# Optimization experiments

Measured on AMD Instinct MI355X. Metric: run time of the kernel, lower is better.

The kernel has to match this reference:

```python
import jax, jax.numpy as jnp
import numpy as np

SIGMA = 1.5
KSIZE = 3
CROP = 5

def _gaussian_window():
    # matches cv2.getGaussianKernel(3, 1.5): normalized 1D gaussian, outer product
    g = np.exp(-((np.arange(KSIZE) - (KSIZE - 1) / 2.0) ** 2) / (2.0 * SIGMA ** 2))
    g = g / g.sum()
    return np.outer(g, g)  # (3, 3)

def _filt(img, win):
    # img: [B, W, H, C]; 3x3 depthwise correlation with BORDER_REFLECT_101 (= jnp 'reflect')
    C = img.shape[-1]
    p = jnp.pad(img, ((0, 0), (1, 1), (1, 1), (0, 0)), mode='reflect')
    k = jnp.broadcast_to(win[:, :, None, None], (KSIZE, KSIZE, 1, C)).astype(img.dtype)
    return jax.lax.conv_general_dilated(
        p, k, window_strides=(1, 1), padding='VALID',
        dimension_numbers=('NHWC', 'HWIO', 'NHWC'), feature_group_count=C)

def setup_inputs() -> dict:
    key = jax.random.key(0)
    k1, k2 = jax.random.split(key)
    X = jax.random.uniform(k1, (32, 3, 512, 512), dtype=jnp.float32) * 255.0
    Y = jax.random.uniform(k2, (32, 3, 512, 512), dtype=jnp.float32) * 255.0
    return {"X": X, "Y": Y}

def reference(X, Y):
    B, C, W, H = X.shape
    # source does numpy reshape (c,w,h)->(w,h,c); replicate exactly
    x = X.reshape(B, W, H, C)
    y = Y.reshape(B, W, H, C)
    win = jnp.asarray(_gaussian_window(), dtype=X.dtype)
    c = slice(CROP, -CROP)
    mu1 = _filt(x, win)[:, c, c, :]
    mu2 = _filt(y, win)[:, c, c, :]
    sigma1_sq = _filt(x * x, win)[:, c, c, :] - mu1 * mu1
    sigma2_sq = _filt(y * y, win)[:, c, c, :] - mu2 * mu2
    sigma12 = _filt(x * y, win)[:, c, c, :] - mu1 * mu2
    loss = sigma1_sq + sigma2_sq - 2.0 * sigma12  # local variance of (x - y)
    return jnp.sum(jnp.mean(loss, axis=(1, 2, 3)))
```

## Files before the change

kernel.cpp:

```cpp
#include <hip/hip_runtime.h>


constexpr int Wd     = 512;
constexpr int Hd     = 512;
constexpr int Cd     = 3;
constexpr int ROW    = Hd * Cd;
constexpr int CROPc  = 5;
constexpr int NOUTc  = Wd - 2 * CROPc;
constexpr int HC_LO  = 15;
constexpr int HC_HI  = 1520;

constexpr int NWIN   = 7;
constexpr int OUTW   = 246;
constexpr int NCHUNK = 24;
constexpr int CHUNKc = 21;
constexpr int BLOCK  = 256;
constexpr int NWAVES = 32 * NCHUNK * NWIN;
constexpr int NBLK   = NWAVES / (BLOCK / 64);
static_assert(NWAVES % (BLOCK / 64) == 0, "");

__global__ __launch_bounds__(BLOCK) void locvar_kernel(
    const float* __restrict__ X,
    const float* __restrict__ Y,
    float* __restrict__ partial)
{
    const int lane = threadIdx.x & 63;
    const int widx = threadIdx.x >> 6;
    const int gw   = blockIdx.x * (BLOCK / 64) + widx;

    const int win   = gw % NWIN;
    const int rest  = gw / NWIN;
    const int chunk = rest % NCHUNK;
    const int b     = rest / NCHUNK;

    const int o_lo = HC_LO + OUTW * win;
    const int o_hi = min(o_lo + OUTW - 1, HC_HI);
    const int s    = (o_lo - 3) & ~3;
    const int idx0 = s + 4 * lane;

    const int w0 = CROPc + chunk * CHUNKc;
    const int wn = min(CHUNKc, CROPc + NOUTc - w0);

    float4 msk;
    msk.x = (idx0 + 0 >= o_lo && idx0 + 0 <= o_hi) ? 1.0f : 0.0f;
    msk.y = (idx0 + 1 >= o_lo && idx0 + 1 <= o_hi) ? 1.0f : 0.0f;
    msk.z = (idx0 + 2 >= o_lo && idx0 + 2 <= o_hi) ? 1.0f : 0.0f;
    msk.w = (idx0 + 3 >= o_lo && idx0 + 3 <= o_hi) ? 1.0f : 0.0f;

    const float e  = expf(-1.0f / 4.5f);
    const float g1 = 1.0f / (1.0f + 2.0f * e);
    const float g0 = e * g1;

    const int am = ((lane - 1) & 63) << 2;
    const int ap = ((lane + 1) & 63) << 2;

    const size_t base = (size_t)b * Wd * ROW + (size_t)idx0;

#define BPERM(A, V) __int_as_float(__builtin_amdgcn_ds_bpermute((A), __float_as_int(V)))

#define ROWSUMS(OFF, Rr, Qq)                                                   \
    {                                                                          \
        float4 x4 = *reinterpret_cast<const float4*>(X + (OFF));               \
        float4 y4 = *reinterpret_cast<const float4*>(Y + (OFF));               \
        float4 d;                                                              \
        d.x = x4.x - y4.x; d.y = x4.y - y4.y;                                  \
        d.z = x4.z - y4.z; d.w = x4.w - y4.w;                                  \
        float pm1 = BPERM(am, d.y), pm2 = BPERM(am, d.z), pm3 = BPERM(am, d.w);\
        float np0 = BPERM(ap, d.x), np1 = BPERM(ap, d.y), np2 = BPERM(ap, d.z);\
        float4 dm, dp;                                                         \
        dm.x = pm1; dm.y = pm2; dm.z = pm3; dm.w = d.x;                        \
        dp.x = d.w; dp.y = np0; dp.z = np1; dp.w = np2;                        \
        Rr.x = fmaf(g0, dm.x + dp.x, g1 * d.x);                                \
        Rr.y = fmaf(g0, dm.y + dp.y, g1 * d.y);                                \
        Rr.z = fmaf(g0, dm.z + dp.z, g1 * d.z);                                \
        Rr.w = fmaf(g0, dm.w + dp.w, g1 * d.w);                                \
        Qq.x = fmaf(g0, fmaf(dp.x, dp.x, dm.x * dm.x), g1 * (d.x * d.x));      \
        Qq.y = fmaf(g0, fmaf(dp.y, dp.y, dm.y * dm.y), g1 * (d.y * d.y));      \
        Qq.z = fmaf(g0, fmaf(dp.z, dp.z, dm.z * dm.z), g1 * (d.z * d.z));      \
        Qq.w = fmaf(g0, fmaf(dp.w, dp.w, dm.w * dm.w), g1 * (d.w * d.w));      \
    }

    float4 R0, R1, Q0, Q1;
    {
        size_t off = base + (size_t)(w0 - 1) * ROW;
        ROWSUMS(off, R0, Q0);
        off += ROW;
        ROWSUMS(off, R1, Q1);
    }

    float4 acc = {0.0f, 0.0f, 0.0f, 0.0f};
    size_t off = base + (size_t)(w0 + 1) * ROW;
    #pragma unroll 3
    for (int i = 0; i < wn; ++i, off += ROW) {
        float4 R2, Q2;
        ROWSUMS(off, R2, Q2);

        float4 S1, S2;
        S1.x = fmaf(g0, R0.x + R2.x, g1 * R1.x);
        S1.y = fmaf(g0, R0.y + R2.y, g1 * R1.y);
        S1.z = fmaf(g0, R0.z + R2.z, g1 * R1.z);
        S1.w = fmaf(g0, R0.w + R2.w, g1 * R1.w);
        S2.x = fmaf(g0, Q0.x + Q2.x, g1 * Q1.x);
        S2.y = fmaf(g0, Q0.y + Q2.y, g1 * Q1.y);
        S2.z = fmaf(g0, Q0.z + Q2.z, g1 * Q1.z);
        S2.w = fmaf(g0, Q0.w + Q2.w, g1 * Q1.w);

        acc.x = fmaf(msk.x, fmaf(-S1.x, S1.x, S2.x), acc.x);
        acc.y = fmaf(msk.y, fmaf(-S1.y, S1.y, S2.y), acc.y);
        acc.z = fmaf(msk.z, fmaf(-S1.z, S1.z, S2.z), acc.z);
        acc.w = fmaf(msk.w, fmaf(-S1.w, S1.w, S2.w), acc.w);

        R0 = R1; R1 = R2;
        Q0 = Q1; Q1 = Q2;
    }
#undef ROWSUMS
#undef BPERM

    float a = (acc.x + acc.y) + (acc.z + acc.w);

    #pragma unroll
    for (int o = 32; o > 0; o >>= 1) a += __shfl_down(a, o, 64);

    __shared__ float sdata[BLOCK / 64];
    if (lane == 0) sdata[widx] = a;
    __syncthreads();
    if (threadIdx.x == 0) {
        float sum = 0.0f;
        #pragma unroll
        for (int i = 0; i < BLOCK / 64; ++i) sum += sdata[i];
        partial[blockIdx.x] = sum;
    }
}

__global__ __launch_bounds__(BLOCK) void reduce_kernel(
    const float* __restrict__ partial,
    float* __restrict__ out)
{
    float acc = 0.0f;
    for (int i = threadIdx.x; i < NBLK; i += BLOCK) acc += partial[i];

    #pragma unroll
    for (int o = 32; o > 0; o >>= 1) acc += __shfl_down(acc, o, 64);

    __shared__ float sdata[BLOCK / 64];
    const int lane = threadIdx.x & 63;
    const int wid  = threadIdx.x >> 6;
    if (lane == 0) sdata[wid] = acc;
    __syncthreads();
    if (threadIdx.x == 0) {
        float s = 0.0f;
        #pragma unroll
        for (int i = 0; i < BLOCK / 64; ++i) s += sdata[i];
        out[0] = s * (1.0f / ((float)NOUTc * (float)NOUTc * (float)Cd));
    }
}

extern "C" void kernel_launch(void* const* d_in, const int* in_sizes, int n_in,
                              void* d_out, int out_size, void* d_ws, size_t ws_size,
                              hipStream_t stream) {
    const float* X = (const float*)d_in[0];
    const float* Y = (const float*)d_in[1];
    float* out     = (float*)d_out;
    float* partial = (float*)d_ws;

    locvar_kernel<<<NBLK, BLOCK, 0, stream>>>(X, Y, partial);
    reduce_kernel<<<1, BLOCK, 0, stream>>>(partial, out);
}
```

Measured before the change: 45.17 us.

## Prefetch next row in registers, shrink row chunks, set occupancy hint

```diff
diff --git a/kernel.cpp b/kernel.cpp
--- a/kernel.cpp
+++ b/kernel.cpp
@@ -12,14 +12,14 @@
 
 constexpr int NWIN   = 7;
 constexpr int OUTW   = 246;
-constexpr int NCHUNK = 24;
-constexpr int CHUNKc = 21;
+constexpr int NCHUNK = 32;
+constexpr int CHUNKc = 16;
 constexpr int BLOCK  = 256;
 constexpr int NWAVES = 32 * NCHUNK * NWIN;
 constexpr int NBLK   = NWAVES / (BLOCK / 64);
 static_assert(NWAVES % (BLOCK / 64) == 0, "");
 
-__global__ __launch_bounds__(BLOCK) void locvar_kernel(
+__global__ __launch_bounds__(BLOCK, 6) void locvar_kernel(
     const float* __restrict__ X,
     const float* __restrict__ Y,
     float* __restrict__ partial)
@@ -58,10 +58,8 @@
 
 #define BPERM(A, V) __int_as_float(__builtin_amdgcn_ds_bpermute((A), __float_as_int(V)))
 
-#define ROWSUMS(OFF, Rr, Qq)                                                   \
+#define ROWSUMS_REG(x4, y4, Rr, Qq)                                            \
     {                                                                          \
-        float4 x4 = *reinterpret_cast<const float4*>(X + (OFF));               \
-        float4 y4 = *reinterpret_cast<const float4*>(Y + (OFF));               \
         float4 d;                                                              \
         d.x = x4.x - y4.x; d.y = x4.y - y4.y;                                  \
         d.z = x4.z - y4.z; d.w = x4.w - y4.w;                                  \
@@ -81,19 +79,31 @@
     }
 
     float4 R0, R1, Q0, Q1;
+    float4 xc, yc;
+    size_t off = base + (size_t)(w0 - 1) * ROW;
     {
-        size_t off = base + (size_t)(w0 - 1) * ROW;
-        ROWSUMS(off, R0, Q0);
-        off += ROW;
-        ROWSUMS(off, R1, Q1);
+        float4 xa = *reinterpret_cast<const float4*>(X + off);
+        float4 ya = *reinterpret_cast<const float4*>(Y + off);
+        float4 xb = *reinterpret_cast<const float4*>(X + off + ROW);
+        float4 yb = *reinterpret_cast<const float4*>(Y + off + ROW);
+        xc = *reinterpret_cast<const float4*>(X + off + 2 * ROW);
+        yc = *reinterpret_cast<const float4*>(Y + off + 2 * ROW);
+        ROWSUMS_REG(xa, ya, R0, Q0);
+        ROWSUMS_REG(xb, yb, R1, Q1);
     }
+    off += 3 * (size_t)ROW;
 
     float4 acc = {0.0f, 0.0f, 0.0f, 0.0f};
-    size_t off = base + (size_t)(w0 + 1) * ROW;
-    #pragma unroll 3
+    #pragma unroll 2
     for (int i = 0; i < wn; ++i, off += ROW) {
+        float4 xn, yn;
+        if (i + 1 < wn) {
+            xn = *reinterpret_cast<const float4*>(X + off);
+            yn = *reinterpret_cast<const float4*>(Y + off);
+        }
+
         float4 R2, Q2;
-        ROWSUMS(off, R2, Q2);
+        ROWSUMS_REG(xc, yc, R2, Q2);
 
         float4 S1, S2;
         S1.x = fmaf(g0, R0.x + R2.x, g1 * R1.x);
@@ -112,8 +122,9 @@
 
         R0 = R1; R1 = R2;
         Q0 = Q1; Q1 = Q2;
+        xc = xn; yc = yn;
     }
-#undef ROWSUMS
+#undef ROWSUMS_REG
 #undef BPERM
 
     float a = (acc.x + acc.y) + (acc.z + acc.w);
```

After: 44.76 us. No clear change (-0.9%).
